# Kernel optimization log

Measured on AMD Instinct MI355X. Metric: run time of the kernel, lower is better.

The kernel has to match this reference:

```python
import jax, jax.numpy as jnp
import numpy as np

HID, NBINS = 256, 4
NMIR, NMRNA, B, NP, PD = 2000, 20000, 16, 2048, 1024
EREG, EPM, EPI = 300000, 320000, 32000


def _lin(x, w, b):
    return x @ w.T + b


def _gelu(x):
    # torch nn.GELU default = exact erf formulation
    return jax.nn.gelu(x, approximate=False)


def _ln(x, g, b):
    m = jnp.mean(x, axis=-1, keepdims=True)
    v = jnp.mean((x - m) ** 2, axis=-1, keepdims=True)
    return (x - m) * jax.lax.rsqrt(v + 1e-5) * g + b


def setup_inputs() -> dict:
    key = jax.random.key(0)
    ks = jax.random.split(key, 48)

    def lin_w(i, dout, din):
        s = 1.0 / np.sqrt(din)
        return jax.random.uniform(ks[i], (dout, din), minval=-s, maxval=s, dtype=jnp.float32)

    inp = {}
    inp['emb_mirna'] = jax.random.normal(ks[0], (NMIR, HID), jnp.float32) * 0.02
    inp['emb_mrna'] = jax.random.normal(ks[1], (NMRNA, HID), jnp.float32) * 0.02
    inp['w_mir2mrna'] = jax.random.uniform(ks[2], (EREG,), jnp.float32)
    inp['w_mrna2mir'] = jax.random.uniform(ks[3], (EREG,), jnp.float32)
    inp['w_mrna2pat'] = jax.random.uniform(ks[4], (EPM,), jnp.float32)
    inp['w_mir2pat'] = jax.random.uniform(ks[5], (EPI,), jnp.float32)
    inp['reg_w_mrna'] = lin_w(6, HID, HID)
    inp['reg_b_mrna'] = jnp.zeros((HID,), jnp.float32)
    inp['reg_w_mirna'] = lin_w(7, HID, HID)
    inp['reg_b_mirna'] = jnp.zeros((HID,), jnp.float32)
    inp['proj_w'] = lin_w(8, HID, HID)
    inp['proj_b'] = jnp.zeros((HID,), jnp.float32)
    inp['ln_g'] = jnp.ones((HID,), jnp.float32)
    inp['ln_b'] = jnp.zeros((HID,), jnp.float32)
    inp['omics_w'] = lin_w(9, NBINS, HID)
    inp['omics_b'] = jnp.zeros((NBINS,), jnp.float32)
    inp['wsi_w'] = lin_w(10, HID, PD)
    inp['wsi_b'] = jnp.zeros((HID,), jnp.float32)
    inp['mlp_w'] = lin_w(11, HID, HID)
    inp['mlp_b'] = jnp.zeros((HID,), jnp.float32)
    inp['wln_g'] = jnp.ones((HID,), jnp.float32)
    inp['wln_b'] = jnp.zeros((HID,), jnp.float32)
    inp['fuse_w1'] = lin_w(12, HID, 2 * HID)
    inp['fuse_b1'] = jnp.zeros((HID,), jnp.float32)
    inp['fuse_w2'] = lin_w(13, NBINS, HID)
    inp['fuse_b2'] = jnp.zeros((NBINS,), jnp.float32)
    inp['patches'] = jax.random.normal(ks[14], (B, NP, PD), jnp.float32)
    inp['mask'] = jnp.ones((B, NP), jnp.float32)
    inp['src_mir2mrna'] = jax.random.randint(ks[15], (EREG,), 0, NMIR, jnp.int32)
    inp['dst_mir2mrna'] = jax.random.randint(ks[16], (EREG,), 0, NMRNA, jnp.int32)
    inp['src_mrna2mir'] = jax.random.randint(ks[17], (EREG,), 0, NMRNA, jnp.int32)
    inp['dst_mrna2mir'] = jax.random.randint(ks[18], (EREG,), 0, NMIR, jnp.int32)
    inp['src_mrna2pat'] = jax.random.randint(ks[19], (EPM,), 0, NMRNA, jnp.int32)
    inp['dst_mrna2pat'] = jax.random.randint(ks[20], (EPM,), 0, B, jnp.int32)
    inp['src_mir2pat'] = jax.random.randint(ks[21], (EPI,), 0, NMIR, jnp.int32)
    inp['dst_mir2pat'] = jax.random.randint(ks[22], (EPI,), 0, B, jnp.int32)
    return inp


def reference(emb_mirna, emb_mrna, w_mir2mrna, w_mrna2mir, w_mrna2pat, w_mir2pat,
              reg_w_mrna, reg_b_mrna, reg_w_mirna, reg_b_mirna,
              proj_w, proj_b, ln_g, ln_b, omics_w, omics_b,
              wsi_w, wsi_b, mlp_w, mlp_b, wln_g, wln_b,
              fuse_w1, fuse_b1, fuse_w2, fuse_b2, patches, mask,
              src_mir2mrna, dst_mir2mrna, src_mrna2mir, dst_mrna2mir,
              src_mrna2pat, dst_mrna2pat, src_mir2pat, dst_mir2pat):
    # ---- omics: node embeddings (nid = arange -> full tables) ----
    h_mir, h_mrna = emb_mirna, emb_mrna
    # ---- SimpleRegEncoder: weighted gather-scatter-sum per etype (on ORIGINAL h) ----
    agg_mrna = jax.ops.segment_sum(h_mir[src_mir2mrna] * w_mir2mrna[:, None], dst_mir2mrna, num_segments=NMRNA)
    agg_mir = jax.ops.segment_sum(h_mrna[src_mrna2mir] * w_mrna2mir[:, None], dst_mrna2mir, num_segments=NMIR)
    h_mrna = h_mrna + _gelu(_lin(agg_mrna, reg_w_mrna, reg_b_mrna))  # dropout = identity (eval)
    h_mir = h_mir + _gelu(_lin(agg_mir, reg_w_mirna, reg_b_mirna))
    # ---- PatientReadout: cross_reducer='sum' over both gene->patient etypes ----
    acc = (jax.ops.segment_sum(h_mrna[src_mrna2pat] * w_mrna2pat[:, None], dst_mrna2pat, num_segments=B)
           + jax.ops.segment_sum(h_mir[src_mir2pat] * w_mir2pat[:, None], dst_mir2pat, num_segments=B))
    pat = _ln(_gelu(_lin(acc, proj_w, proj_b)), ln_g, ln_b)  # [B, HID]
    omics_logits = _lin(pat, omics_w, omics_b)  # [B, NBINS]
    # ---- SimpleWSIEncoder ----
    x = _lin(patches, wsi_w, wsi_b)  # [B, NP, HID]
    denom = jnp.clip(jnp.sum(mask, axis=1, keepdims=True), 1.0, None)
    pooled = jnp.sum(x * mask[:, :, None], axis=1) / denom
    pooled = _gelu(_lin(_gelu(pooled), mlp_w, mlp_b))
    wsi = _ln(pooled, wln_g, wln_b)  # [B, HID]
    # ---- fusion head ----
    cat = jnp.concatenate([pat, wsi], axis=-1)  # [B, 2*HID]
    fused = _lin(_gelu(_lin(cat, fuse_w1, fuse_b1)), fuse_w2, fuse_b2)  # [B, NBINS]
    return fused, omics_logits
```

## Files before the change

kernel.cpp:

```cpp
#include <hip/hip_runtime.h>
#include <math.h>

#define HID 256
#define NBINS 4
#define NMIR 2000
#define NMRNA 20000
#define NG (NMRNA + NMIR)
#define BB 16
#define NP 2048
#define PD 1024
#define EREG 300000
#define EPM 320000
#define EPI 32000

typedef __attribute__((ext_vector_type(8))) short bf16x8;
typedef __attribute__((ext_vector_type(4))) float f32x4;

__device__ __forceinline__ float gelu_exact(float x) {
    return 0.5f * x * (1.0f + erff(x * 0.7071067811865475f));
}

__device__ __forceinline__ unsigned short f2b(float f) {
    union { float f; unsigned int u; } v; v.f = f;
    unsigned int u = v.u + 0x7fffu + ((v.u >> 16) & 1u);
    return (unsigned short)(u >> 16);
}

__device__ __forceinline__ float b2f(unsigned short u) {
    union { unsigned int i; float f; } v; v.i = ((unsigned int)u) << 16;
    return v.f;
}

__device__ __forceinline__ float block_reduce_sum(float v, float* red) {
    int c = threadIdx.x;
    red[c] = v;
    __syncthreads();
    for (int st = 128; st > 0; st >>= 1) {
        if (c < st) red[c] += red[c + st];
        __syncthreads();
    }
    float r = red[0];
    __syncthreads();
    return r;
}

__device__ __forceinline__ float kred(float v, float* red, int b, int kk) {
    red[kk * 16 + b] = v;
    __syncthreads();
    for (int st = 8; st >= 1; st >>= 1) {
        if (kk < st) red[kk * 16 + b] += red[(kk + st) * 16 + b];
        __syncthreads();
    }
    float r = red[b];
    __syncthreads();
    return r;
}

#define M3_EMB ((NG * HID) / 4096)
#define M3_F2B ((2 * HID * HID) / 4096)
#define M3_HIST ((2 * EREG + 2047) / 2048)
#define M3_WSC ((EPM + EPI + 2047) / 2048)
#define M3_TOTAL (M3_EMB + M3_F2B + M3_HIST + M3_WSC)

__global__ __launch_bounds__(256) void k_misc3(
        const float* __restrict__ emb_mirna, const float* __restrict__ emb_mrna,
        unsigned short* __restrict__ embB_mir, unsigned short* __restrict__ embB_mrna,
        const float* __restrict__ regwA, const float* __restrict__ regwB,
        unsigned short* __restrict__ wb,
        const int* __restrict__ dA, const int* __restrict__ dB, int* __restrict__ cnt,
        const int* __restrict__ srcP, const int* __restrict__ dstP, const float* __restrict__ wP,
        const int* __restrict__ srcI, const int* __restrict__ dstI, const float* __restrict__ wI,
        float* __restrict__ Wp) {
    int bid = blockIdx.x;
    int t = threadIdx.x;
    if (bid < M3_EMB) {
        const size_t NM = (size_t)NMIR * HID;
        float4 v[4];
#pragma unroll
        for (int k = 0; k < 4; k++) {
            size_t e = (size_t)bid * 4096 + k * 1024 + t * 4;
            v[k] = (e < NM) ? *(const float4*)(emb_mirna + e)
                            : *(const float4*)(emb_mrna + (e - NM));
        }
#pragma unroll
        for (int k = 0; k < 4; k++) {
            size_t e = (size_t)bid * 4096 + k * 1024 + t * 4;
            ushort4 u = { f2b(v[k].x), f2b(v[k].y), f2b(v[k].z), f2b(v[k].w) };
            if (e < NM) *(ushort4*)(embB_mir + e) = u;
            else        *(ushort4*)(embB_mrna + (e - NM)) = u;
        }
        return;
    }
    bid -= M3_EMB;
    if (bid < M3_F2B) {
        const size_t NW = (size_t)HID * HID;
        float4 v[4];
#pragma unroll
        for (int k = 0; k < 4; k++) {
            size_t e = (size_t)bid * 4096 + k * 1024 + t * 4;
            v[k] = (e < NW) ? *(const float4*)(regwA + e)
                            : *(const float4*)(regwB + (e - NW));
        }
#pragma unroll
        for (int k = 0; k < 4; k++) {
            size_t e = (size_t)bid * 4096 + k * 1024 + t * 4;
            ushort4 u = { f2b(v[k].x), f2b(v[k].y), f2b(v[k].z), f2b(v[k].w) };
            *(ushort4*)(wb + e) = u;
        }
        return;
    }
    bid -= M3_F2B;
    if (bid < M3_HIST) {
        int base = bid * 2048 + t;
        int dd[8];
#pragma unroll
        for (int k = 0; k < 8; k++) {
            int i = base + k * 256;
            dd[k] = -1;
            if (i < EREG) dd[k] = dA[i];
            else if (i < 2 * EREG) dd[k] = NMRNA + dB[i - EREG];
        }
#pragma unroll
        for (int k = 0; k < 8; k++)
            if (dd[k] >= 0) atomicAdd(&cnt[dd[k]], 1);
        return;
    }
    bid -= M3_HIST;
    {
        int base = bid * 2048 + t;
        int addr[8];
        float val[8];
#pragma unroll
        for (int k = 0; k < 8; k++) {
            int i = base + k * 256;
            addr[k] = -1;
            if (i < EPM) {
                addr[k] = dstP[i] * NG + srcP[i];
                val[k] = wP[i];
            } else if (i < EPM + EPI) {
                int j = i - EPM;
                addr[k] = dstI[j] * NG + NMRNA + srcI[j];
                val[k] = wI[j];
            }
        }
#pragma unroll
        for (int k = 0; k < 8; k++)
            if (addr[k] >= 0) atomicAdd(&Wp[addr[k]], val[k]);
    }
}

#define PSLICES 128
#define PCHUNK (NP / PSLICES)
__global__ __launch_bounds__(256) void k_pool(
        const float* __restrict__ patches, const float* __restrict__ mask,
        float* __restrict__ pooled, float* __restrict__ masksum) {
    int b = blockIdx.y;
    int p0 = blockIdx.x * PCHUNK;
    int t = threadIdx.x;
    float4 acc = {0.f, 0.f, 0.f, 0.f};
    float msum = 0.f;
#pragma unroll
    for (int pp = 0; pp < PCHUNK; pp++) {
        int p = p0 + pp;
        float m = mask[b * NP + p];
        float4 v = ((const float4*)(patches + ((size_t)b * NP + p) * PD))[t];
        msum += m;
        acc.x += m * v.x; acc.y += m * v.y; acc.z += m * v.z; acc.w += m * v.w;
    }
    float* op = pooled + (size_t)b * PD + t * 4;
    atomicAdd(op + 0, acc.x);
    atomicAdd(op + 1, acc.y);
    atomicAdd(op + 2, acc.z);
    atomicAdd(op + 3, acc.w);
    if (t == 0) atomicAdd(&masksum[b], msum);
}

__global__ __launch_bounds__(1024) void k_scan2(const int* __restrict__ cnt,
                                                int* __restrict__ rpA, int* __restrict__ cuA,
                                                int* __restrict__ rpB, int* __restrict__ cuB) {
    __shared__ int part[1024];
    const int* c = (blockIdx.x == 0) ? cnt : cnt + NMRNA;
    int n = (blockIdx.x == 0) ? NMRNA : NMIR;
    int* rowptr = (blockIdx.x == 0) ? rpA : rpB;
    int* cursor = (blockIdx.x == 0) ? cuA : cuB;
    int t = threadIdx.x;
    int chunk = (n + 1023) >> 10;
    int beg = t * chunk;
    int end = min(beg + chunk, n);
    int s = 0;
    for (int i = beg; i < end; i++) s += c[i];
    part[t] = s;
    __syncthreads();
    for (int st = 1; st < 1024; st <<= 1) {
        int v = (t >= st) ? part[t - st] : 0;
        __syncthreads();
        part[t] += v;
        __syncthreads();
    }
    int off = part[t] - s;
    for (int i = beg; i < end; i++) {
        rowptr[i] = off;
        cursor[i] = off;
        off += c[i];
    }
    if (end == n) rowptr[n] = off;
}

#define PLACE_B ((EREG + 1023) / 1024)
__global__ __launch_bounds__(256) void k_place3(
        const int* __restrict__ srcA, const int* __restrict__ dstA, const float* __restrict__ wA,
        int* __restrict__ cuA, int2* __restrict__ epA,
        const int* __restrict__ srcB, const int* __restrict__ dstB, const float* __restrict__ wB,
        int* __restrict__ cuB, int2* __restrict__ epB) {
    int bid = blockIdx.x;
    int t = threadIdx.x;
    const int* src; const int* dst; const float* w; int* cu; int2* epp;
    if (bid < PLACE_B) { src = srcA; dst = dstA; w = wA; cu = cuA; epp = epA; }
    else { bid -= PLACE_B; src = srcB; dst = dstB; w = wB; cu = cuB; epp = epB; }
    int base = bid * 1024 + t;
    int dd[4], ss[4];
    float ww[4];
#pragma unroll
    for (int k = 0; k < 4; k++) {
        int i = base + k * 256;
        dd[k] = -1;
        if (i < EREG) { dd[k] = dst[i]; ss[k] = src[i]; ww[k] = w[i]; }
    }
#pragma unroll
    for (int k = 0; k < 4; k++) {
        if (dd[k] >= 0) {
            int p = atomicAdd(&cu[dd[k]], 1);
            int2 e; e.x = ss[k]; e.y = __float_as_int(ww[k]);
            epp[p] = e;
        }
    }
}

__global__ __launch_bounds__(256) void k_gather2(
        const unsigned short* __restrict__ embB_mir, const unsigned short* __restrict__ embB_mrna,
        const int* __restrict__ rpA, const int2* __restrict__ epA,
        const int* __restrict__ rpB, const int2* __restrict__ epB,
        unsigned short* __restrict__ agg) {
    __shared__ float lacc[4][HID];
    int n = blockIdx.x;
    const unsigned short* emb;
    const int* rp; const int2* ep;
    int node;
    if (n < NMRNA) { emb = embB_mir;  rp = rpA; ep = epA; node = n; }
    else           { emb = embB_mrna; rp = rpB; ep = epB; node = n - NMRNA; }
    int wv = threadIdx.x >> 6, l = threadIdx.x & 63;
    int beg = rp[node], end = rp[node + 1];
    float a0 = 0.f, a1 = 0.f, a2 = 0.f, a3 = 0.f;
    float c0 = 0.f, c1 = 0.f, c2 = 0.f, c3 = 0.f;
    float d0 = 0.f, d1 = 0.f, d2 = 0.f, d3 = 0.f;
    float g0 = 0.f, g1 = 0.f, g2 = 0.f, g3 = 0.f;
    int j = beg + wv;
    for (; j + 12 < end; j += 16) {
        int2 e0 = ep[j];
        int2 e1 = ep[j + 4];
        int2 e2 = ep[j + 8];
        int2 e3 = ep[j + 12];
        float w0 = __int_as_float(e0.y), w1 = __int_as_float(e1.y);
        float w2 = __int_as_float(e2.y), w3 = __int_as_float(e3.y);
        ushort4 v0 = *(const ushort4*)(emb + (size_t)e0.x * HID + l * 4);
        ushort4 v1 = *(const ushort4*)(emb + (size_t)e1.x * HID + l * 4);
        ushort4 v2 = *(const ushort4*)(emb + (size_t)e2.x * HID + l * 4);
        ushort4 v3 = *(const ushort4*)(emb + (size_t)e3.x * HID + l * 4);
        a0 += w0 * b2f(v0.x); a1 += w0 * b2f(v0.y); a2 += w0 * b2f(v0.z); a3 += w0 * b2f(v0.w);
        c0 += w1 * b2f(v1.x); c1 += w1 * b2f(v1.y); c2 += w1 * b2f(v1.z); c3 += w1 * b2f(v1.w);
        d0 += w2 * b2f(v2.x); d1 += w2 * b2f(v2.y); d2 += w2 * b2f(v2.z); d3 += w2 * b2f(v2.w);
        g0 += w3 * b2f(v3.x); g1 += w3 * b2f(v3.y); g2 += w3 * b2f(v3.z); g3 += w3 * b2f(v3.w);
    }
    for (; j < end; j += 4) {
        int2 e0 = ep[j];
        float w0 = __int_as_float(e0.y);
        ushort4 v0 = *(const ushort4*)(emb + (size_t)e0.x * HID + l * 4);
        a0 += w0 * b2f(v0.x); a1 += w0 * b2f(v0.y); a2 += w0 * b2f(v0.z); a3 += w0 * b2f(v0.w);
    }
    float4 st = { a0 + c0 + d0 + g0, a1 + c1 + d1 + g1,
                  a2 + c2 + d2 + g2, a3 + c3 + d3 + g3 };
    ((float4*)lacc[wv])[l] = st;
    __syncthreads();
    int c = threadIdx.x;
    agg[(size_t)n * HID + c] = f2b(lacc[0][c] + lacc[1][c] + lacc[2][c] + lacc[3][c]);
}

__global__ __launch_bounds__(256) void k_update2(
        const unsigned short* __restrict__ A,
        const float* __restrict__ emb_mrna, const float* __restrict__ emb_mirna,
        const unsigned short* __restrict__ wb,
        const float* __restrict__ bias_mrna, const float* __restrict__ bias_mirna,
        const float* __restrict__ Wp, float* __restrict__ acc_pat) {
    __shared__ float ht[16][HID + 1];
    int row0 = blockIdx.x * 16;
    const float* emb; const unsigned short* Wb; const float* bias; int base;
    if (row0 < NMRNA) { emb = emb_mrna;  Wb = wb;             bias = bias_mrna;  base = 0; }
    else              { emb = emb_mirna; Wb = wb + HID * HID; bias = bias_mirna; base = NMRNA; }
    int wv = threadIdx.x >> 6;
    int lane = threadIdx.x & 63;
    int m = lane & 15;
    int q = lane >> 4;
    bf16x8 afrag[8];
    const unsigned short* arow = A + (size_t)(row0 + m) * HID + q * 8;
#pragma unroll
    for (int kk = 0; kk < 8; kk++)
        afrag[kk] = *(const bf16x8*)(arow + kk * 32);
    f32x4 acc[4];
#pragma unroll
    for (int t = 0; t < 4; t++) acc[t] = (f32x4){0.f, 0.f, 0.f, 0.f};
    int col_base = wv * 64;
#pragma unroll
    for (int t = 0; t < 4; t++) {
        const unsigned short* brow = Wb + (size_t)(col_base + t * 16 + m) * HID + q * 8;
#pragma unroll
        for (int kk = 0; kk < 8; kk++) {
            bf16x8 bfrag = *(const bf16x8*)(brow + kk * 32);
            acc[t] = __builtin_amdgcn_mfma_f32_16x16x32_bf16(afrag[kk], bfrag, acc[t], 0, 0, 0);
        }
    }
#pragma unroll
    for (int t = 0; t < 4; t++) {
        int col = col_base + t * 16 + m;
        float bv = bias[col];
#pragma unroll
        for (int r = 0; r < 4; r++) {
            int lrow = q * 4 + r;
            size_t idxe = (size_t)(row0 - base + lrow) * HID + col;
            ht[lrow][col] = emb[idxe] + gelu_exact(acc[t][r] + bv);
        }
    }
    __syncthreads();
    int c = threadIdx.x;
    float hv[16];
#pragma unroll
    for (int r = 0; r < 16; r++) hv[r] = ht[r][c];
#pragma unroll
    for (int b = 0; b < BB; b++) {
        const float* wpr = Wp + (size_t)b * NG + row0;
        float s = 0.f;
#pragma unroll
        for (int r = 0; r < 16; r++) s += wpr[r] * hv[r];
        atomicAdd(&acc_pat[b * HID + c], s);
    }
}

__global__ __launch_bounds__(256) void k_head_a(
        const float* __restrict__ acc_pat, const float* __restrict__ pooled,
        const float* __restrict__ masksum,
        const float* __restrict__ proj_w, const float* __restrict__ proj_b,
        const float* __restrict__ wsi_w, const float* __restrict__ wsi_b,
        float* __restrict__ pg, float* __restrict__ wt) {
    __shared__ float red[256];
    int c = blockIdx.x;
    int t = threadIdx.x;
    int b = t & 15, kk = t >> 4;

    const float* wr = proj_w + (size_t)c * HID + kk * 16;
    const float* xr = acc_pat + (size_t)b * HID + kk * 16;
    float s = 0.f;
#pragma unroll
    for (int i = 0; i < 16; i += 4) {
        float4 w4 = *(const float4*)(wr + i);
        float4 x4 = *(const float4*)(xr + i);
        s += x4.x * w4.x + x4.y * w4.y + x4.z * w4.z + x4.w * w4.w;
    }
    float tot = kred(s, red, b, kk);
    if (kk == 0) pg[(size_t)b * HID + c] = gelu_exact(tot + proj_b[c]);

    const float* wr2 = wsi_w + (size_t)c * PD + kk * 64;
    const float* xr2 = pooled + (size_t)b * PD + kk * 64;
    float s2 = 0.f;
#pragma unroll
    for (int i = 0; i < 64; i += 4) {
        float4 w4 = *(const float4*)(wr2 + i);
        float4 x4 = *(const float4*)(xr2 + i);
        s2 += x4.x * w4.x + x4.y * w4.y + x4.z * w4.z + x4.w * w4.w;
    }
    float tot2 = kred(s2, red, b, kk);
    if (kk == 0) {
        float sm = masksum[b];
        float denom = fmaxf(sm, 1.0f);
        wt[(size_t)b * HID + c] = gelu_exact(tot2 / denom + wsi_b[c] * (sm / denom));
    }
}

__global__ __launch_bounds__(256) void k_head_b(
        const float* __restrict__ wt,
        const float* __restrict__ mlp_w, const float* __restrict__ mlp_b,
        float* __restrict__ ml) {
    __shared__ float red[256];
    int c = blockIdx.x;
    int t = threadIdx.x;
    int b = t & 15, kk = t >> 4;
    const float* wr = mlp_w + (size_t)c * HID + kk * 16;
    const float* xr = wt + (size_t)b * HID + kk * 16;
    float s = 0.f;
#pragma unroll
    for (int i = 0; i < 16; i += 4) {
        float4 w4 = *(const float4*)(wr + i);
        float4 x4 = *(const float4*)(xr + i);
        s += x4.x * w4.x + x4.y * w4.y + x4.z * w4.z + x4.w * w4.w;
    }
    float tot = kred(s, red, b, kk);
    if (kk == 0) ml[(size_t)b * HID + c] = gelu_exact(tot + mlp_b[c]);
}

__global__ __launch_bounds__(256) void k_head_c(
        const float* __restrict__ pg, const float* __restrict__ ml,
        const float* __restrict__ ln_g, const float* __restrict__ ln_b,
        const float* __restrict__ wln_g, const float* __restrict__ wln_b,
        const float* __restrict__ omics_w, const float* __restrict__ omics_b,
        const float* __restrict__ fuse_b2,
        float* __restrict__ vecbuf, float* __restrict__ out_omics,
        float* __restrict__ out_fused) {
    __shared__ float red[256];
    int b = blockIdx.x, c = threadIdx.x;
    if (c < NBINS) out_fused[b * NBINS + c] = fuse_b2[c];
    float g = pg[(size_t)b * HID + c];
    float mean = block_reduce_sum(g, red) * (1.0f / HID);
    float d = g - mean;
    float var = block_reduce_sum(d * d, red) * (1.0f / HID);
    float patv = d * rsqrtf(var + 1e-5f) * ln_g[c] + ln_b[c];
    vecbuf[(size_t)b * (2 * HID) + c] = patv;
    for (int o = 0; o < NBINS; o++) {
        float r = block_reduce_sum(patv * omics_w[o * HID + c], red);
        if (c == 0) out_omics[b * NBINS + o] = r + omics_b[o];
    }
    float m = ml[(size_t)b * HID + c];
    mean = block_reduce_sum(m, red) * (1.0f / HID);
    d = m - mean;
    var = block_reduce_sum(d * d, red) * (1.0f / HID);
    vecbuf[(size_t)b * (2 * HID) + HID + c] = d * rsqrtf(var + 1e-5f) * wln_g[c] + wln_b[c];
}

__global__ __launch_bounds__(256) void k_head_d(
        const float* __restrict__ vecbuf,
        const float* __restrict__ fuse_w1, const float* __restrict__ fuse_b1,
        const float* __restrict__ fuse_w2,
        float* __restrict__ out_fused) {
    __shared__ float red[256];
    int c = blockIdx.x;
    int t = threadIdx.x;
    int b = t & 15, kk = t >> 4;
    const float* wr = fuse_w1 + (size_t)c * (2 * HID) + kk * 32;
    const float* xr = vecbuf + (size_t)b * (2 * HID) + kk * 32;
    float s = 0.f;
#pragma unroll
    for (int i = 0; i < 32; i += 4) {
        float4 w4 = *(const float4*)(wr + i);
        float4 x4 = *(const float4*)(xr + i);
        s += x4.x * w4.x + x4.y * w4.y + x4.z * w4.z + x4.w * w4.w;
    }
    float tot = kred(s, red, b, kk);
    if (kk == 0) {
        float h1 = gelu_exact(tot + fuse_b1[c]);
#pragma unroll
        for (int o = 0; o < NBINS; o++)
            atomicAdd(&out_fused[b * NBINS + o], h1 * fuse_w2[o * HID + c]);
    }
}

extern "C" void kernel_launch(void* const* d_in, const int* in_sizes, int n_in,
                              void* d_out, int out_size, void* d_ws, size_t ws_size,
                              hipStream_t stream) {
    const float* emb_mirna  = (const float*)d_in[0];
    const float* emb_mrna   = (const float*)d_in[1];
    const float* w_mir2mrna = (const float*)d_in[2];
    const float* w_mrna2mir = (const float*)d_in[3];
    const float* w_mrna2pat = (const float*)d_in[4];
    const float* w_mir2pat  = (const float*)d_in[5];
    const float* reg_w_mrna = (const float*)d_in[6];
    const float* reg_b_mrna = (const float*)d_in[7];
    const float* reg_w_mirna= (const float*)d_in[8];
    const float* reg_b_mirna= (const float*)d_in[9];
    const float* proj_w     = (const float*)d_in[10];
    const float* proj_b     = (const float*)d_in[11];
    const float* ln_g       = (const float*)d_in[12];
    const float* ln_b       = (const float*)d_in[13];
    const float* omics_w    = (const float*)d_in[14];
    const float* omics_b    = (const float*)d_in[15];
    const float* wsi_w      = (const float*)d_in[16];
    const float* wsi_b      = (const float*)d_in[17];
    const float* mlp_w      = (const float*)d_in[18];
    const float* mlp_b      = (const float*)d_in[19];
    const float* wln_g      = (const float*)d_in[20];
    const float* wln_b      = (const float*)d_in[21];
    const float* fuse_w1    = (const float*)d_in[22];
    const float* fuse_b1    = (const float*)d_in[23];
    const float* fuse_w2    = (const float*)d_in[24];
    const float* fuse_b2    = (const float*)d_in[25];
    const float* patches    = (const float*)d_in[26];
    const float* mask       = (const float*)d_in[27];
    const int* src_m2M = (const int*)d_in[28];
    const int* dst_m2M = (const int*)d_in[29];
    const int* src_M2m = (const int*)d_in[30];
    const int* dst_M2m = (const int*)d_in[31];
    const int* src_M2p = (const int*)d_in[32];
    const int* dst_M2p = (const int*)d_in[33];
    const int* src_m2p = (const int*)d_in[34];
    const int* dst_m2p = (const int*)d_in[35];

    float* ws = (float*)d_ws;
    size_t off = 0;
    float* acc_pat  = ws + off; off += (size_t)BB * HID;
    float* pooled   = ws + off; off += (size_t)BB * PD;
    float* Wp       = ws + off; off += (size_t)BB * NG;
    int* cnt        = (int*)(ws + off); off += NG;
    float* masksum  = ws + off; off += BB;
    size_t zero_floats = off;
    unsigned short* agg_bf = (unsigned short*)(ws + off); off += (size_t)NG * HID / 2;
    unsigned short* wb     = (unsigned short*)(ws + off); off += (size_t)2 * HID * HID / 2;
    unsigned short* embB_mir  = (unsigned short*)(ws + off); off += (size_t)NMIR * HID / 2;
    unsigned short* embB_mrna = (unsigned short*)(ws + off); off += (size_t)NMRNA * HID / 2;
    float* pg       = ws + off; off += (size_t)BB * HID;
    float* wt       = ws + off; off += (size_t)BB * HID;
    float* ml       = ws + off; off += (size_t)BB * HID;
    float* vecbuf   = ws + off; off += (size_t)BB * 2 * HID;
    int2* epA       = (int2*)(ws + off); off += (size_t)2 * EREG;
    int2* epB       = (int2*)(ws + off); off += (size_t)2 * EREG;
    int* rowptr_A   = (int*)(ws + off); off += NMRNA + 1;
    int* cursor_A   = (int*)(ws + off); off += NMRNA;
    int* rowptr_B   = (int*)(ws + off); off += NMIR + 1;
    int* cursor_B   = (int*)(ws + off); off += NMIR;

    float* out_fused = (float*)d_out;
    float* out_omics = (float*)d_out + BB * NBINS;

    hipMemsetAsync(d_ws, 0, zero_floats * sizeof(float), stream);

    k_misc3<<<M3_TOTAL, 256, 0, stream>>>(
        emb_mirna, emb_mrna, embB_mir, embB_mrna,
        reg_w_mrna, reg_w_mirna, wb,
        dst_m2M, dst_M2m, cnt,
        src_M2p, dst_M2p, w_mrna2pat, src_m2p, dst_m2p, w_mir2pat, Wp);

    k_pool<<<dim3(PSLICES, BB), 256, 0, stream>>>(patches, mask, pooled, masksum);

    k_scan2<<<2, 1024, 0, stream>>>(cnt, rowptr_A, cursor_A, rowptr_B, cursor_B);
    k_place3<<<2 * PLACE_B, 256, 0, stream>>>(
        src_m2M, dst_m2M, w_mir2mrna, cursor_A, epA,
        src_M2m, dst_M2m, w_mrna2mir, cursor_B, epB);

    k_gather2<<<NG, 256, 0, stream>>>(embB_mir, embB_mrna,
                                      rowptr_A, epA, rowptr_B, epB, agg_bf);

    k_update2<<<NG / 16, 256, 0, stream>>>(agg_bf, emb_mrna, emb_mirna, wb,
                                           reg_b_mrna, reg_b_mirna, Wp, acc_pat);

    k_head_a<<<HID, 256, 0, stream>>>(acc_pat, pooled, masksum,
                                      proj_w, proj_b, wsi_w, wsi_b, pg, wt);
    k_head_b<<<HID, 256, 0, stream>>>(wt, mlp_w, mlp_b, ml);
    k_head_c<<<BB, 256, 0, stream>>>(pg, ml, ln_g, ln_b, wln_g, wln_b,
                                     omics_w, omics_b, fuse_b2,
                                     vecbuf, out_omics, out_fused);
    k_head_d<<<HID, 256, 0, stream>>>(vecbuf, fuse_w1, fuse_b1, fuse_w2, out_fused);
}
```

Baseline: 607.4 us.

## Replace global-atomic histogram and dense patient matrix with blocked LDS counting sort

Edge bucketing now runs as a blocked counting sort: a few large blocks build per-block histograms in shared memory, a scan produces per-block base offsets, and a placement pass uses shared-memory cursors. This replaces the many global atomics used for counting and placement. The dense BB x NG patient weight matrix, filled by global float atomics, becomes a CSR of gene-to-patient edges that each update block reduces into a small shared tile. The cost is that histogram and placement now run on only 24 blocks, which limits parallelism and adds an extra histogram-merging scan, while global atomic contention and the zeroing of the dense matrix go away.

Measured after the change: 995.6 us. 1.64x slower.

```diff
diff --git a/kernel.cpp b/kernel.cpp
--- a/kernel.cpp
+++ b/kernel.cpp
@@ -56,24 +56,18 @@
     return r;
 }
 
-#define M3_EMB ((NG * HID) / 4096)
-#define M3_F2B ((2 * HID * HID) / 4096)
-#define M3_HIST ((2 * EREG + 2047) / 2048)
-#define M3_WSC ((EPM + EPI + 2047) / 2048)
-#define M3_TOTAL (M3_EMB + M3_F2B + M3_HIST + M3_WSC)
-
-__global__ __launch_bounds__(256) void k_misc3(
+#define CVT_EMB ((NG * HID) / 4096)
+#define CVT_F2B ((2 * HID * HID) / 4096)
+#define CVT_TOTAL (CVT_EMB + CVT_F2B)
+
+__global__ __launch_bounds__(256) void k_cvt(
         const float* __restrict__ emb_mirna, const float* __restrict__ emb_mrna,
         unsigned short* __restrict__ embB_mir, unsigned short* __restrict__ embB_mrna,
         const float* __restrict__ regwA, const float* __restrict__ regwB,
-        unsigned short* __restrict__ wb,
-        const int* __restrict__ dA, const int* __restrict__ dB, int* __restrict__ cnt,
-        const int* __restrict__ srcP, const int* __restrict__ dstP, const float* __restrict__ wP,
-        const int* __restrict__ srcI, const int* __restrict__ dstI, const float* __restrict__ wI,
-        float* __restrict__ Wp) {
+        unsigned short* __restrict__ wb) {
     int bid = blockIdx.x;
     int t = threadIdx.x;
-    if (bid < M3_EMB) {
+    if (bid < CVT_EMB) {
         const size_t NM = (size_t)NMIR * HID;
         float4 v[4];
 #pragma unroll
@@ -91,8 +85,8 @@
         }
         return;
     }
-    bid -= M3_EMB;
-    if (bid < M3_F2B) {
+    bid -= CVT_EMB;
+    {
         const size_t NW = (size_t)HID * HID;
         float4 v[4];
 #pragma unroll
@@ -107,45 +101,120 @@
             ushort4 u = { f2b(v[k].x), f2b(v[k].y), f2b(v[k].z), f2b(v[k].w) };
             *(ushort4*)(wb + e) = u;
         }
-        return;
-    }
-    bid -= M3_F2B;
-    if (bid < M3_HIST) {
-        int base = bid * 2048 + t;
-        int dd[8];
-#pragma unroll
-        for (int k = 0; k < 8; k++) {
-            int i = base + k * 256;
-            dd[k] = -1;
-            if (i < EREG) dd[k] = dA[i];
-            else if (i < 2 * EREG) dd[k] = NMRNA + dB[i - EREG];
-        }
-#pragma unroll
-        for (int k = 0; k < 8; k++)
-            if (dd[k] >= 0) atomicAdd(&cnt[dd[k]], 1);
-        return;
-    }
-    bid -= M3_HIST;
-    {
-        int base = bid * 2048 + t;
-        int addr[8];
-        float val[8];
-#pragma unroll
-        for (int k = 0; k < 8; k++) {
-            int i = base + k * 256;
-            addr[k] = -1;
-            if (i < EPM) {
-                addr[k] = dstP[i] * NG + srcP[i];
-                val[k] = wP[i];
-            } else if (i < EPM + EPI) {
-                int j = i - EPM;
-                addr[k] = dstI[j] * NG + NMRNA + srcI[j];
-                val[k] = wI[j];
-            }
-        }
-#pragma unroll
-        for (int k = 0; k < 8; k++)
-            if (addr[k] >= 0) atomicAdd(&Wp[addr[k]], val[k]);
+    }
+}
+
+#define NBR 16
+#define NBP 8
+#define PER_R ((2 * EREG + NBR - 1) / NBR)
+#define PER_P ((EPM + EPI + NBP - 1) / NBP)
+
+__global__ __launch_bounds__(1024) void k_hist(
+        const int* __restrict__ dR1, const int* __restrict__ dR2,
+        const int* __restrict__ sP1, const int* __restrict__ sP2,
+        int* __restrict__ histR, int* __restrict__ histP) {
+    __shared__ int lh[NG];
+    int t = threadIdx.x, bid = blockIdx.x;
+    for (int i = t; i < NG; i += 1024) lh[i] = 0;
+    __syncthreads();
+    if (bid < NBR) {
+        int beg = bid * PER_R, end = min(beg + PER_R, 2 * EREG);
+        for (int i = beg + t; i < end; i += 1024) {
+            int d = (i < EREG) ? dR1[i] : NMRNA + dR2[i - EREG];
+            atomicAdd(&lh[d], 1);
+        }
+        __syncthreads();
+        int* out = histR + (size_t)bid * NG;
+        for (int i = t; i < NG; i += 1024) out[i] = lh[i];
+    } else {
+        int pb = bid - NBR;
+        int beg = pb * PER_P, end = min(beg + PER_P, EPM + EPI);
+        for (int i = beg + t; i < end; i += 1024) {
+            int g = (i < EPM) ? sP1[i] : NMRNA + sP2[i - EPM];
+            atomicAdd(&lh[g], 1);
+        }
+        __syncthreads();
+        int* out = histP + (size_t)pb * NG;
+        for (int i = t; i < NG; i += 1024) out[i] = lh[i];
+    }
+}
+
+__global__ __launch_bounds__(1024) void k_scan(
+        const int* __restrict__ histR, const int* __restrict__ histP,
+        int* __restrict__ rowptrR, int* __restrict__ baseR,
+        int* __restrict__ rowptrP, int* __restrict__ baseP) {
+    __shared__ int part[1024];
+    int isP = blockIdx.x;
+    const int* hist = isP ? histP : histR;
+    int nb = isP ? NBP : NBR;
+    int* rowptr = isP ? rowptrP : rowptrR;
+    int* base = isP ? baseP : baseR;
+    int t = threadIdx.x;
+    const int chunk = (NG + 1023) >> 10;
+    int beg = t * chunk, end = min(beg + chunk, NG);
+    int s = 0;
+    for (int i = beg; i < end; i++) {
+        int c = 0;
+        for (int b = 0; b < nb; b++) c += hist[(size_t)b * NG + i];
+        s += c;
+    }
+    part[t] = s;
+    __syncthreads();
+    for (int st = 1; st < 1024; st <<= 1) {
+        int v = (t >= st) ? part[t - st] : 0;
+        __syncthreads();
+        part[t] += v;
+        __syncthreads();
+    }
+    int off = part[t] - s;
+    for (int i = beg; i < end; i++) {
+        rowptr[i] = off;
+        int acc = off;
+        for (int b = 0; b < nb; b++) {
+            base[(size_t)b * NG + i] = acc;
+            acc += hist[(size_t)b * NG + i];
+        }
+        off = acc;
+    }
+    if (end == NG) rowptr[NG] = off;
+}
+
+__global__ __launch_bounds__(1024) void k_place(
+        const int* __restrict__ sR1, const int* __restrict__ dR1, const float* __restrict__ wR1,
+        const int* __restrict__ sR2, const int* __restrict__ dR2, const float* __restrict__ wR2,
+        const int* __restrict__ sP1, const int* __restrict__ dP1, const float* __restrict__ wP1,
+        const int* __restrict__ sP2, const int* __restrict__ dP2, const float* __restrict__ wP2,
+        const int* __restrict__ baseR, const int* __restrict__ baseP,
+        int2* __restrict__ epR, int2* __restrict__ epP) {
+    __shared__ int lcur[NG];
+    int t = threadIdx.x, bid = blockIdx.x;
+    if (bid < NBR) {
+        const int* base = baseR + (size_t)bid * NG;
+        for (int i = t; i < NG; i += 1024) lcur[i] = base[i];
+        __syncthreads();
+        int beg = bid * PER_R, end = min(beg + PER_R, 2 * EREG);
+        for (int i = beg + t; i < end; i += 1024) {
+            int d, s; float w;
+            if (i < EREG) { d = dR1[i]; s = sR1[i]; w = wR1[i]; }
+            else { int k = i - EREG; d = NMRNA + dR2[k]; s = sR2[k]; w = wR2[k]; }
+            int p = atomicAdd(&lcur[d], 1);
+            int2 e; e.x = s; e.y = __float_as_int(w);
+            epR[p] = e;
+        }
+    } else {
+        int pb = bid - NBR;
+        const int* base = baseP + (size_t)pb * NG;
+        for (int i = t; i < NG; i += 1024) lcur[i] = base[i];
+        __syncthreads();
+        int beg = pb * PER_P, end = min(beg + PER_P, EPM + EPI);
+        for (int i = beg + t; i < end; i += 1024) {
+            int g, b; float w;
+            if (i < EPM) { g = sP1[i]; b = dP1[i]; w = wP1[i]; }
+            else { int k = i - EPM; g = NMRNA + sP2[k]; b = dP2[k]; w = wP2[k]; }
+            int p = atomicAdd(&lcur[g], 1);
+            int2 e; e.x = (g << 4) | b; e.y = __float_as_int(w);
+            epP[p] = e;
+        }
     }
 }
 
@@ -175,91 +244,25 @@
     if (t == 0) atomicAdd(&masksum[b], msum);
 }
 
-__global__ __launch_bounds__(1024) void k_scan2(const int* __restrict__ cnt,
-                                                int* __restrict__ rpA, int* __restrict__ cuA,
-                                                int* __restrict__ rpB, int* __restrict__ cuB) {
-    __shared__ int part[1024];
-    const int* c = (blockIdx.x == 0) ? cnt : cnt + NMRNA;
-    int n = (blockIdx.x == 0) ? NMRNA : NMIR;
-    int* rowptr = (blockIdx.x == 0) ? rpA : rpB;
-    int* cursor = (blockIdx.x == 0) ? cuA : cuB;
-    int t = threadIdx.x;
-    int chunk = (n + 1023) >> 10;
-    int beg = t * chunk;
-    int end = min(beg + chunk, n);
-    int s = 0;
-    for (int i = beg; i < end; i++) s += c[i];
-    part[t] = s;
-    __syncthreads();
-    for (int st = 1; st < 1024; st <<= 1) {
-        int v = (t >= st) ? part[t - st] : 0;
-        __syncthreads();
-        part[t] += v;
-        __syncthreads();
-    }
-    int off = part[t] - s;
-    for (int i = beg; i < end; i++) {
-        rowptr[i] = off;
-        cursor[i] = off;
-        off += c[i];
-    }
-    if (end == n) rowptr[n] = off;
-}
-
-#define PLACE_B ((EREG + 1023) / 1024)
-__global__ __launch_bounds__(256) void k_place3(
-        const int* __restrict__ srcA, const int* __restrict__ dstA, const float* __restrict__ wA,
-        int* __restrict__ cuA, int2* __restrict__ epA,
-        const int* __restrict__ srcB, const int* __restrict__ dstB, const float* __restrict__ wB,
-        int* __restrict__ cuB, int2* __restrict__ epB) {
-    int bid = blockIdx.x;
-    int t = threadIdx.x;
-    const int* src; const int* dst; const float* w; int* cu; int2* epp;
-    if (bid < PLACE_B) { src = srcA; dst = dstA; w = wA; cu = cuA; epp = epA; }
-    else { bid -= PLACE_B; src = srcB; dst = dstB; w = wB; cu = cuB; epp = epB; }
-    int base = bid * 1024 + t;
-    int dd[4], ss[4];
-    float ww[4];
-#pragma unroll
-    for (int k = 0; k < 4; k++) {
-        int i = base + k * 256;
-        dd[k] = -1;
-        if (i < EREG) { dd[k] = dst[i]; ss[k] = src[i]; ww[k] = w[i]; }
-    }
-#pragma unroll
-    for (int k = 0; k < 4; k++) {
-        if (dd[k] >= 0) {
-            int p = atomicAdd(&cu[dd[k]], 1);
-            int2 e; e.x = ss[k]; e.y = __float_as_int(ww[k]);
-            epp[p] = e;
-        }
-    }
-}
-
 __global__ __launch_bounds__(256) void k_gather2(
         const unsigned short* __restrict__ embB_mir, const unsigned short* __restrict__ embB_mrna,
-        const int* __restrict__ rpA, const int2* __restrict__ epA,
-        const int* __restrict__ rpB, const int2* __restrict__ epB,
+        const int* __restrict__ rowptrR, const int2* __restrict__ epR,
         unsigned short* __restrict__ agg) {
     __shared__ float lacc[4][HID];
     int n = blockIdx.x;
-    const unsigned short* emb;
-    const int* rp; const int2* ep;
-    int node;
-    if (n < NMRNA) { emb = embB_mir;  rp = rpA; ep = epA; node = n; }
-    else           { emb = embB_mrna; rp = rpB; ep = epB; node = n - NMRNA; }
+    const unsigned short* emb = (n < NMRNA) ? embB_mir : embB_mrna;
     int wv = threadIdx.x >> 6, l = threadIdx.x & 63;
-    int beg = rp[node], end = rp[node + 1];
+    int beg = rowptrR[n], end = rowptrR[n + 1];
     float a0 = 0.f, a1 = 0.f, a2 = 0.f, a3 = 0.f;
     float c0 = 0.f, c1 = 0.f, c2 = 0.f, c3 = 0.f;
     float d0 = 0.f, d1 = 0.f, d2 = 0.f, d3 = 0.f;
     float g0 = 0.f, g1 = 0.f, g2 = 0.f, g3 = 0.f;
     int j = beg + wv;
     for (; j + 12 < end; j += 16) {
-        int2 e0 = ep[j];
-        int2 e1 = ep[j + 4];
-        int2 e2 = ep[j + 8];
-        int2 e3 = ep[j + 12];
+        int2 e0 = epR[j];
+        int2 e1 = epR[j + 4];
+        int2 e2 = epR[j + 8];
+        int2 e3 = epR[j + 12];
         float w0 = __int_as_float(e0.y), w1 = __int_as_float(e1.y);
         float w2 = __int_as_float(e2.y), w3 = __int_as_float(e3.y);
         ushort4 v0 = *(const ushort4*)(emb + (size_t)e0.x * HID + l * 4);
@@ -272,7 +275,7 @@
         g0 += w3 * b2f(v3.x); g1 += w3 * b2f(v3.y); g2 += w3 * b2f(v3.z); g3 += w3 * b2f(v3.w);
     }
     for (; j < end; j += 4) {
-        int2 e0 = ep[j];
+        int2 e0 = epR[j];
         float w0 = __int_as_float(e0.y);
         ushort4 v0 = *(const ushort4*)(emb + (size_t)e0.x * HID + l * 4);
         a0 += w0 * b2f(v0.x); a1 += w0 * b2f(v0.y); a2 += w0 * b2f(v0.z); a3 += w0 * b2f(v0.w);
@@ -290,14 +293,24 @@
         const float* __restrict__ emb_mrna, const float* __restrict__ emb_mirna,
         const unsigned short* __restrict__ wb,
         const float* __restrict__ bias_mrna, const float* __restrict__ bias_mirna,
-        const float* __restrict__ Wp, float* __restrict__ acc_pat) {
+        const int* __restrict__ rowptrP, const int2* __restrict__ epP,
+        float* __restrict__ acc_pat) {
     __shared__ float ht[16][HID + 1];
+    __shared__ float wtile[16][BB];
     int row0 = blockIdx.x * 16;
     const float* emb; const unsigned short* Wb; const float* bias; int base;
     if (row0 < NMRNA) { emb = emb_mrna;  Wb = wb;             bias = bias_mrna;  base = 0; }
     else              { emb = emb_mirna; Wb = wb + HID * HID; bias = bias_mirna; base = NMRNA; }
-    int wv = threadIdx.x >> 6;
-    int lane = threadIdx.x & 63;
+    int tid = threadIdx.x;
+    if (tid < 16 * BB) wtile[tid >> 4][tid & 15] = 0.f;
+    __syncthreads();
+    int pbeg = rowptrP[row0], pend = rowptrP[row0 + 16];
+    for (int j = pbeg + tid; j < pend; j += 256) {
+        int2 e = epP[j];
+        atomicAdd(&wtile[(e.x >> 4) - row0][e.x & 15], __int_as_float(e.y));
+    }
+    int wv = tid >> 6;
+    int lane = tid & 63;
     int m = lane & 15;
     int q = lane >> 4;
     bf16x8 afrag[8];
@@ -330,16 +343,15 @@
         }
     }
     __syncthreads();
-    int c = threadIdx.x;
+    int c = tid;
     float hv[16];
 #pragma unroll
     for (int r = 0; r < 16; r++) hv[r] = ht[r][c];
 #pragma unroll
     for (int b = 0; b < BB; b++) {
-        const float* wpr = Wp + (size_t)b * NG + row0;
         float s = 0.f;
 #pragma unroll
-        for (int r = 0; r < 16; r++) s += wpr[r] * hv[r];
+        for (int r = 0; r < 16; r++) s += wtile[r][b] * hv[r];
         atomicAdd(&acc_pat[b * HID + c], s);
     }
 }
@@ -504,8 +516,6 @@
     size_t off = 0;
     float* acc_pat  = ws + off; off += (size_t)BB * HID;
     float* pooled   = ws + off; off += (size_t)BB * PD;
-    float* Wp       = ws + off; off += (size_t)BB * NG;
-    int* cnt        = (int*)(ws + off); off += NG;
     float* masksum  = ws + off; off += BB;
     size_t zero_floats = off;
     unsigned short* agg_bf = (unsigned short*)(ws + off); off += (size_t)NG * HID / 2;
@@ -516,36 +526,39 @@
     float* wt       = ws + off; off += (size_t)BB * HID;
     float* ml       = ws + off; off += (size_t)BB * HID;
     float* vecbuf   = ws + off; off += (size_t)BB * 2 * HID;
-    int2* epA       = (int2*)(ws + off); off += (size_t)2 * EREG;
-    int2* epB       = (int2*)(ws + off); off += (size_t)2 * EREG;
-    int* rowptr_A   = (int*)(ws + off); off += NMRNA + 1;
-    int* cursor_A   = (int*)(ws + off); off += NMRNA;
-    int* rowptr_B   = (int*)(ws + off); off += NMIR + 1;
-    int* cursor_B   = (int*)(ws + off); off += NMIR;
+    int* histR      = (int*)(ws + off); off += (size_t)NBR * NG;
+    int* histP      = (int*)(ws + off); off += (size_t)NBP * NG;
+    int* baseR      = (int*)(ws + off); off += (size_t)NBR * NG;
+    int* baseP      = (int*)(ws + off); off += (size_t)NBP * NG;
+    int* rowptrR    = (int*)(ws + off); off += NG + 2;
+    int* rowptrP    = (int*)(ws + off); off += NG + 2;
+    int2* epR       = (int2*)(ws + off); off += (size_t)2 * (2 * EREG);
+    int2* epP       = (int2*)(ws + off); off += (size_t)2 * (EPM + EPI);
 
     float* out_fused = (float*)d_out;
     float* out_omics = (float*)d_out + BB * NBINS;
 
     hipMemsetAsync(d_ws, 0, zero_floats * sizeof(float), stream);
 
-    k_misc3<<<M3_TOTAL, 256, 0, stream>>>(
+    k_cvt<<<CVT_TOTAL, 256, 0, stream>>>(
         emb_mirna, emb_mrna, embB_mir, embB_mrna,
-        reg_w_mrna, reg_w_mirna, wb,
-        dst_m2M, dst_M2m, cnt,
-        src_M2p, dst_M2p, w_mrna2pat, src_m2p, dst_m2p, w_mir2pat, Wp);
+        reg_w_mrna, reg_w_mirna, wb);
+
+    k_hist<<<NBR + NBP, 1024, 0, stream>>>(
+        dst_m2M, dst_M2m, src_M2p, src_m2p, histR, histP);
+    k_scan<<<2, 1024, 0, stream>>>(histR, histP, rowptrR, baseR, rowptrP, baseP);
+    k_place<<<NBR + NBP, 1024, 0, stream>>>(
+        src_m2M, dst_m2M, w_mir2mrna, src_M2m, dst_M2m, w_mrna2mir,
+        src_M2p, dst_M2p, w_mrna2pat, src_m2p, dst_m2p, w_mir2pat,
+        baseR, baseP, epR, epP);
 
     k_pool<<<dim3(PSLICES, BB), 256, 0, stream>>>(patches, mask, pooled, masksum);
 
-    k_scan2<<<2, 1024, 0, stream>>>(cnt, rowptr_A, cursor_A, rowptr_B, cursor_B);
-    k_place3<<<2 * PLACE_B, 256, 0, stream>>>(
-        src_m2M, dst_m2M, w_mir2mrna, cursor_A, epA,
-        src_M2m, dst_M2m, w_mrna2mir, cursor_B, epB);
-
-    k_gather2<<<NG, 256, 0, stream>>>(embB_mir, embB_mrna,
-                                      rowptr_A, epA, rowptr_B, epB, agg_bf);
+    k_gather2<<<NG, 256, 0, stream>>>(embB_mir, embB_mrna, rowptrR, epR, agg_bf);
 
     k_update2<<<NG / 16, 256, 0, stream>>>(agg_bf, emb_mrna, emb_mirna, wb,
-                                           reg_b_mrna, reg_b_mirna, Wp, acc_pat);
+                                           reg_b_mrna, reg_b_mirna,
+                                           rowptrP, epP, acc_pat);
 
     k_head_a<<<HID, 256, 0, stream>>>(acc_pat, pooled, masksum,
                                       proj_w, proj_b, wsi_w, wsi_b, pg, wt);
```
